# Kernel optimization log

Hardware: AMD Instinct MI355X
Metric: run time of the kernel (lower is better)

Reference implementation:

```python
import jax, jax.numpy as jnp
import numpy as np

# Module hyperparameters (from init_kwargs)
K = 1.0                       # init_curvature (registered buffer, non-trainable)
HOPFIELD_DIM = 64
BETA = 1.0 / np.sqrt(float(HOPFIELD_DIM))  # beta=None default -> 1/sqrt(d_h)
EPS = 1e-7

# ---- Lorentz / hyperboloid ops (geoopt conventions, curvature param k>0) ----

def _to_tangent0(x):
    # x: (..., d) Euclidean -> (..., d+1) in T_0 H via [0, x], norm-clipped to 3.5
    zeros = jnp.zeros(x.shape[:-1] + (1,), x.dtype)
    x = jnp.concatenate([zeros, x], axis=-1)
    n = jnp.linalg.norm(x, axis=-1, keepdims=True)
    factor = jnp.minimum(3.5 / (n + 1e-7), 1.0)
    return x * factor

def expmap0(x_euc):
    # (..., d) Euclidean -> (..., d+1) on hyperboloid via Exp_0([0, x])
    u = _to_tangent0(x_euc)
    x = u[..., 1:]
    sqrtk = jnp.sqrt(K)
    xn = jnp.maximum(jnp.linalg.norm(x, axis=-1, keepdims=True), EPS)
    theta = xn / sqrtk
    return jnp.concatenate(
        [sqrtk * jnp.cosh(theta), sqrtk * jnp.sinh(theta) * x / xn], axis=-1)

def logmap0(y):
    # (..., d+1) on hyperboloid -> (..., d) tangent at origin (spatial part)
    sqrtk = jnp.sqrt(K)
    y0 = y[..., :1]
    yr = y[..., 1:]
    yn = jnp.maximum(jnp.linalg.norm(yr, axis=-1, keepdims=True), EPS)
    d = sqrtk * jnp.arccosh(jnp.maximum(y0 / sqrtk, 1.0 + EPS))
    return d * yr / yn

def minkowski_inner(u, v):
    # <u,v>_L = -u0 v0 + sum_i u_i v_i ; returns (...) without last dim
    return -u[..., 0] * v[..., 0] + jnp.sum(u[..., 1:] * v[..., 1:], axis=-1)

# ---- KFCore forward ----

def _kfcore(queries, keys, values, Wq, bq, Wk, bk, Wv, bv):
    sqrtk = jnp.sqrt(K)
    Qe = queries @ Wq.T + bq                     # (B,S,d_h)
    Ke = keys @ Wk.T + bk                        # (B,M,d_h)
    Ve = (values @ Wk.T + bk) @ Wv.T + bv        # (B,M,d_out)
    Q = expmap0(Qe)                              # (B,S,d+1)
    Kh = expmap0(Ke)                             # (B,M,d+1)
    V = expmap0(Ve)                              # (B,M,d+1)

    dp1 = Q.shape[-1]
    sign = jnp.concatenate([-jnp.ones((1,), Q.dtype), jnp.ones((dp1 - 1,), Q.dtype)])

    # Minkowski inner pairwise: (B,S,M)
    sims = jnp.einsum('bsd,bmd->bsm', Q * sign, Kh)
    alpha = jax.nn.softmax(-BETA * sims, axis=-1)          # (B,S,M)

    # Karcher flow: tangent_mean = sum_m alpha * logmap_Q(V_m)
    # logmap_x(y) = dist(x,y) * (y + (<x,y>/k) x) / ||y + (<x,y>/k) x||_L
    ip = jnp.einsum('bsd,bmd->bsm', Q * sign, V)           # <Q_s, V_m>_L
    dist = sqrtk * jnp.arccosh(jnp.maximum(-ip / K, 1.0 + EPS))
    qq = minkowski_inner(Q, Q)[:, :, None]                 # (B,S,1)
    vv = minkowski_inner(V, V)[:, None, :]                 # (B,1,M)
    c = ip / K
    nomin_sq = vv + 2.0 * c * ip + c * c * qq              # ||nomin||_L^2, (B,S,M)
    denom = jnp.sqrt(jnp.maximum(nomin_sq, EPS))
    w = alpha * dist / denom                               # (B,S,M)
    # sum_m w * (V_m + c * Q_s)  -- avoids the (B,S,M,d+1) logmap tensor
    tm = jnp.einsum('bsm,bmd->bsd', w, V) \
         + jnp.sum(w * c, axis=-1, keepdims=True) * Q      # (B,S,d+1)

    # expmap_Q(tm) = cosh(||tm||/sqrtk) Q + sqrtk sinh(||tm||/sqrtk) tm/||tm||
    un = jnp.sqrt(jnp.maximum(minkowski_inner(tm, tm), EPS))[..., None]
    th = un / sqrtk
    z = jnp.cosh(th) * Q + sqrtk * jnp.sinh(th) * tm / un
    return logmap0(z)                                      # (B,S,d_out)


def setup_inputs() -> dict:
    key = jax.random.key(0)
    ks = jax.random.split(key, 9)
    B, S, M = 2, 2048, 4096
    SD, MD, DH, DO = 256, 256, 64, 64
    sq = 1.0 / np.sqrt(SD)
    sm = 1.0 / np.sqrt(MD)
    sh = 1.0 / np.sqrt(DH)
    return {
        'queries': jax.random.normal(ks[0], (B, S, SD), jnp.float32),
        'keys':    jax.random.normal(ks[1], (B, M, MD), jnp.float32),
        'values':  jax.random.normal(ks[2], (B, M, MD), jnp.float32),
        'Wq': jax.random.normal(ks[3], (DH, SD), jnp.float32) * sq,
        'bq': jax.random.normal(ks[4], (DH,), jnp.float32) * sq,
        'Wk': jax.random.normal(ks[5], (DH, MD), jnp.float32) * sm,
        'bk': jax.random.normal(ks[6], (DH,), jnp.float32) * sm,
        'Wv': jax.random.normal(ks[7], (DO, DH), jnp.float32) * sh,
        'bv': jax.random.normal(ks[8], (DO,), jnp.float32) * sh,
    }


def reference(queries, keys, values, Wq, bq, Wk, bk, Wv, bv):
    return _kfcore(queries, keys, values, Wq, bq, Wk, bk, Wv, bv)
```

## Files before the change

### kernel.cpp

```cpp
#include <hip/hip_runtime.h>
#include <math.h>

#define BETA  0.125f
#define SHIFT 30.0f
#define EPSF  1e-7f

typedef __attribute__((ext_vector_type(8))) short short8;
typedef __attribute__((ext_vector_type(4))) short short4v;
typedef __attribute__((ext_vector_type(4))) float f32x4;

__device__ __forceinline__ unsigned short bf16_rne(float x) {
  unsigned int u = __float_as_uint(x);
  return (unsigned short)((u + 0x7fffu + ((u >> 16) & 1u)) >> 16);
}
__device__ __forceinline__ float bf16_tof(unsigned short h) {
  return __uint_as_float(((unsigned int)h) << 16);
}
__device__ __forceinline__ void split2(float x, unsigned short& h, unsigned short& l) {
  unsigned int u = __float_as_uint(x);
  unsigned int hr = (u + 0x7fffu + ((u >> 16) & 1u)) & 0xffff0000u;
  h = (unsigned short)(hr >> 16);
  l = bf16_rne(x - __uint_as_float(hr));
}

#define ZERO_F4 68608

__global__ __launch_bounds__(256) void proj_kernel(
    const float* __restrict__ Xq, const float* __restrict__ Xk,
    const float* __restrict__ Xv,
    const float* __restrict__ Wq, const float* __restrict__ bq,
    const float* __restrict__ Wk, const float* __restrict__ bk,
    const float* __restrict__ Wv, const float* __restrict__ bv,
    float* __restrict__ Q0, float* __restrict__ K0, float* __restrict__ V0,
    unsigned short* __restrict__ Qh, unsigned short* __restrict__ Ql,
    unsigned short* __restrict__ Kh, unsigned short* __restrict__ Kl,
    unsigned short* __restrict__ Vh, unsigned short* __restrict__ Vl,
    unsigned short* __restrict__ Vth, unsigned short* __restrict__ Vtl,
    float* __restrict__ zeroRegion)
{
  __shared__ float Xs[64 * 64];
  __shared__ float Ws[64 * 64];
  __shared__ unsigned int Tr[64 * 65];

  const int bid = blockIdx.x;
  const int tid = threadIdx.x;

  {
    int idx = bid * 256 + tid;
    if (idx < ZERO_F4)
      *(float4*)&zeroRegion[idx * 4] = make_float4(0.f, 0.f, 0.f, 0.f);
  }

  const float *X, *W, *bias;
  float* y0;
  unsigned short *yh, *yl;
  bool dbl;
  int rowBase;
  if (bid < 128)      { X = Xv; W = Wk; bias = bk; y0 = V0; yh = Vh; yl = Vl; rowBase = bid << 6;         dbl = true;  }
  else if (bid < 256) { X = Xk; W = Wk; bias = bk; y0 = K0; yh = Kh; yl = Kl; rowBase = (bid - 128) << 6; dbl = false; }
  else                { X = Xq; W = Wq; bias = bq; y0 = Q0; yh = Qh; yl = Ql; rowBase = (bid - 256) << 6; dbl = false; }

  const int ty = tid >> 4, tx = tid & 15;
  const int ty4 = ty << 2, tx4 = tx << 2;

  float acc[4][4];
#pragma unroll
  for (int j = 0; j < 4; ++j) {
    float bj = bias[tx4 + j];
#pragma unroll
    for (int i = 0; i < 4; ++i) acc[i][j] = bj;
  }

  for (int kc = 0; kc < 4; ++kc) {
#pragma unroll
    for (int q = 0; q < 4; ++q) {
      int f = tid + (q << 8);
      int r = f >> 4, g = f & 15;
      int sw = (r << 6) + ((g ^ (r >> 2)) << 2);
      *(float4*)&Xs[sw] = *(const float4*)&X[(rowBase + r) * 256 + (kc << 6) + (g << 2)];
      *(float4*)&Ws[sw] = *(const float4*)&W[r * 256 + (kc << 6) + (g << 2)];
    }
    __syncthreads();
#pragma unroll 4
    for (int kk = 0; kk < 64; kk += 4) {
      const int gk = kk >> 2;
      float4 xa[4], wb[4];
#pragma unroll
      for (int i = 0; i < 4; ++i)
        xa[i] = *(const float4*)&Xs[((ty4 + i) << 6) + ((gk ^ ty) << 2)];
#pragma unroll
      for (int j = 0; j < 4; ++j)
        wb[j] = *(const float4*)&Ws[((tx4 + j) << 6) + ((gk ^ tx) << 2)];
#pragma unroll
      for (int i = 0; i < 4; ++i)
#pragma unroll
        for (int j = 0; j < 4; ++j)
          acc[i][j] += xa[i].x * wb[j].x + xa[i].y * wb[j].y +
                       xa[i].z * wb[j].z + xa[i].w * wb[j].w;
    }
    __syncthreads();
  }

  if (dbl) {
#pragma unroll
    for (int i = 0; i < 4; ++i) {
      float4 v = make_float4(acc[i][0], acc[i][1], acc[i][2], acc[i][3]);
      *(float4*)&Xs[((ty4 + i) << 6) + ((tx ^ ty) << 2)] = v;
    }
#pragma unroll
    for (int q = 0; q < 4; ++q) {
      int f = tid + (q << 8);
      int r = f >> 4, g = f & 15;
      int sw = (r << 6) + ((g ^ (r >> 2)) << 2);
      *(float4*)&Ws[sw] = *(const float4*)&Wv[(r << 6) + (g << 2)];
    }
#pragma unroll
    for (int j = 0; j < 4; ++j) {
      float bj = bv[tx4 + j];
#pragma unroll
      for (int i = 0; i < 4; ++i) acc[i][j] = bj;
    }
    __syncthreads();
#pragma unroll 4
    for (int kk = 0; kk < 64; kk += 4) {
      const int gk = kk >> 2;
      float4 xa[4], wb[4];
#pragma unroll
      for (int i = 0; i < 4; ++i)
        xa[i] = *(const float4*)&Xs[((ty4 + i) << 6) + ((gk ^ ty) << 2)];
#pragma unroll
      for (int j = 0; j < 4; ++j)
        wb[j] = *(const float4*)&Ws[((tx4 + j) << 6) + ((gk ^ tx) << 2)];
#pragma unroll
      for (int i = 0; i < 4; ++i)
#pragma unroll
        for (int j = 0; j < 4; ++j)
          acc[i][j] += xa[i].x * wb[j].x + xa[i].y * wb[j].y +
                       xa[i].z * wb[j].z + xa[i].w * wb[j].w;
    }
  }

  float n2p[4];
#pragma unroll
  for (int i = 0; i < 4; ++i)
    n2p[i] = acc[i][0] * acc[i][0] + acc[i][1] * acc[i][1] +
             acc[i][2] * acc[i][2] + acc[i][3] * acc[i][3];
#pragma unroll
  for (int i = 0; i < 4; ++i) {
    n2p[i] += __shfl_xor(n2p[i], 1);
    n2p[i] += __shfl_xor(n2p[i], 2);
    n2p[i] += __shfl_xor(n2p[i], 4);
    n2p[i] += __shfl_xor(n2p[i], 8);
  }
  unsigned short hv[4][4], lv[4][4];
#pragma unroll
  for (int i = 0; i < 4; ++i) {
    float n = sqrtf(n2p[i]);
    float factor = fminf(3.5f / (n + EPSF), 1.0f);
    float xn = fmaxf(n * factor, EPSF);
    float et = __expf(xn);
    float rt = __builtin_amdgcn_rcpf(et);
    float ch = 0.5f * (et + rt);
    float sh = 0.5f * (et - rt);
    float scale = sh * factor * __builtin_amdgcn_rcpf(xn);
    int row = rowBase + ty4 + i;
    if (tx == 0) y0[row] = ch;
#pragma unroll
    for (int j = 0; j < 4; ++j) split2(acc[i][j] * scale, hv[i][j], lv[i][j]);
    unsigned int* ph = (unsigned int*)(yh + row * 64 + tx4);
    ph[0] = (unsigned int)hv[i][0] | ((unsigned int)hv[i][1] << 16);
    ph[1] = (unsigned int)hv[i][2] | ((unsigned int)hv[i][3] << 16);
    unsigned int* pl = (unsigned int*)(yl + row * 64 + tx4);
    pl[0] = (unsigned int)lv[i][0] | ((unsigned int)lv[i][1] << 16);
    pl[1] = (unsigned int)lv[i][2] | ((unsigned int)lv[i][3] << 16);
  }

  if (dbl) {
#pragma unroll
    for (int i = 0; i < 4; ++i)
#pragma unroll
      for (int j = 0; j < 4; ++j)
        Tr[(ty4 + i) * 65 + tx4 + j] = (unsigned int)hv[i][j];
    __syncthreads();
#pragma unroll
    for (int q = 0; q < 2; ++q) {
      int f = tid + (q << 8);
      int d = f >> 3;
      int seg = (f & 7) << 3;
      unsigned int o[4];
#pragma unroll
      for (int k = 0; k < 4; ++k)
        o[k] = Tr[(seg + 2 * k) * 65 + d] | (Tr[(seg + 2 * k + 1) * 65 + d] << 16);
      *(uint4*)&Vth[d * 8192 + rowBase + seg] = make_uint4(o[0], o[1], o[2], o[3]);
    }
    __syncthreads();
#pragma unroll
    for (int i = 0; i < 4; ++i)
#pragma unroll
      for (int j = 0; j < 4; ++j)
        Tr[(ty4 + i) * 65 + tx4 + j] = (unsigned int)lv[i][j];
    __syncthreads();
#pragma unroll
    for (int q = 0; q < 2; ++q) {
      int f = tid + (q << 8);
      int d = f >> 3;
      int seg = (f & 7) << 3;
      unsigned int o[4];
#pragma unroll
      for (int k = 0; k < 4; ++k)
        o[k] = Tr[(seg + 2 * k) * 65 + d] | (Tr[(seg + 2 * k + 1) * 65 + d] << 16);
      *(uint4*)&Vtl[d * 8192 + rowBase + seg] = make_uint4(o[0], o[1], o[2], o[3]);
    }
  }
}

__global__ void __attribute__((amdgpu_waves_per_eu(4)))
__launch_bounds__(256) attn_kernel(
    const float* __restrict__ Q0g, const unsigned short* __restrict__ Qh,
    const unsigned short* __restrict__ Ql,
    const float* __restrict__ K0g, const unsigned short* __restrict__ Khg,
    const unsigned short* __restrict__ Klg,
    const float* __restrict__ V0g, const unsigned short* __restrict__ Vhg,
    const unsigned short* __restrict__ Vlg,
    const unsigned short* __restrict__ Vthg, const unsigned short* __restrict__ Vtlg,
    float* __restrict__ Tacc, float* __restrict__ T0acc,
    float* __restrict__ Lacc, float* __restrict__ WCacc)
{
  __shared__ unsigned short LB[16640];

  const int tid = threadIdx.x;
  const int wave = tid >> 6, lane = tid & 63;
  const int lm = lane & 15;
  const int lg = lane >> 4;
  const int bid = blockIdx.x;
  const int slice = bid & 15;
  const int t = bid >> 4;
  const int b = t >> 5;
  const int sT = t & 31;
  const int sBase = b * 2048 + sT * 64 + wave * 16;

  unsigned short* wbase = LB + 14336 + wave * 576;

  short8 qf[2][2];
#pragma unroll
  for (int ks = 0; ks < 2; ++ks) {
    int idx = (sBase + lm) * 64 + ks * 32 + lg * 8;
    qf[ks][0] = *(const short8*)(Qh + idx);
    qf[ks][1] = *(const short8*)(Ql + idx);
  }
  float q0r[4];
#pragma unroll
  for (int r = 0; r < 4; ++r) q0r[r] = Q0g[sBase + lg * 4 + r];

  f32x4 accT[4];
  float Lp[4], WCp[4], T0p[4];
#pragma unroll
  for (int r = 0; r < 4; ++r) { Lp[r] = 0.f; WCp[r] = 0.f; T0p[r] = 0.f; }
#pragma unroll
  for (int dj = 0; dj < 4; ++dj) accT[dj] = f32x4{0.f, 0.f, 0.f, 0.f};

  const int mSliceBase = b * 4096 + slice * 256;
  const int srow = tid >> 3;
  const int sc8 = (tid & 7) << 3;
  const int drow = tid >> 2;
  const int dseg = (tid & 3) << 3;

  for (int mc = 0; mc < 8; ++mc) {
    const int mCh = mSliceBase + (mc << 5);

    {
      int goff = (mCh + srow) * 64 + sc8;
      int loff = srow * 72 + sc8;
      *(uint4*)&LB[loff]         = *(const uint4*)&Khg[goff];
      *(uint4*)&LB[2304 + loff]  = *(const uint4*)&Klg[goff];
      *(uint4*)&LB[4608 + loff]  = *(const uint4*)&Vhg[goff];
      *(uint4*)&LB[6912 + loff]  = *(const uint4*)&Vlg[goff];
      int gofft = drow * 8192 + mCh + dseg;
      int lofft = drow * 40 + dseg;
      *(uint4*)&LB[9216 + lofft]  = *(const uint4*)&Vthg[gofft];
      *(uint4*)&LB[11776 + lofft] = *(const uint4*)&Vtlg[gofft];
    }
    float k0r[2], v0r[2];
#pragma unroll
    for (int mj = 0; mj < 2; ++mj) {
      k0r[mj] = K0g[mCh + mj * 16 + lm];
      v0r[mj] = V0g[mCh + mj * 16 + lm];
    }
    __syncthreads();

#pragma unroll
    for (int mj = 0; mj < 2; ++mj) {
      f32x4 sims = f32x4{0.f, 0.f, 0.f, 0.f};
      f32x4 ipv  = f32x4{0.f, 0.f, 0.f, 0.f};
#pragma unroll
      for (int ks = 0; ks < 2; ++ks) {
        int off = (mj * 16 + lm) * 72 + ks * 32 + lg * 8;
        short8 kh = *(const short8*)&LB[off];
        short8 kl = *(const short8*)&LB[2304 + off];
        short8 vh = *(const short8*)&LB[4608 + off];
        short8 vl = *(const short8*)&LB[6912 + off];
        sims = __builtin_amdgcn_mfma_f32_16x16x32_bf16(qf[ks][0], kh, sims, 0, 0, 0);
        sims = __builtin_amdgcn_mfma_f32_16x16x32_bf16(qf[ks][0], kl, sims, 0, 0, 0);
        sims = __builtin_amdgcn_mfma_f32_16x16x32_bf16(qf[ks][1], kh, sims, 0, 0, 0);
        ipv  = __builtin_amdgcn_mfma_f32_16x16x32_bf16(qf[ks][0], vh, ipv, 0, 0, 0);
        ipv  = __builtin_amdgcn_mfma_f32_16x16x32_bf16(qf[ks][0], vl, ipv, 0, 0, 0);
        ipv  = __builtin_amdgcn_mfma_f32_16x16x32_bf16(qf[ks][1], vh, ipv, 0, 0, 0);
      }
#pragma unroll
      for (int r = 0; r < 4; ++r) {
        float c  = ipv[r]  - q0r[r] * v0r[mj];
        float sm = sims[r] - q0r[r] * k0r[mj];
        float x = -c;
        float s2 = fmaxf(fmaf(x, x, -1.0f), EPSF);
        float rs = __builtin_amdgcn_rsqf(s2);
        float dist = __logf(fmaf(s2, rs, x));
        float e = __expf(fmaf(-BETA, sm, -SHIFT));
        float w = e * dist * rs;
        unsigned short wu = bf16_rne(w);
        float wb = bf16_tof(wu);
        Lp[r]  += e;
        WCp[r] += wb * c;
        T0p[r] += wb * v0r[mj];
        wbase[(lg * 4 + r) * 36 + mj * 16 + lm] = wu;
      }
    }

    {
      const unsigned short* p = wbase + lm * 36 + lg * 8;
      short4v a0 = *(const short4v*)p;
      short4v a1 = *(const short4v*)(p + 4);
      short8 wa = __builtin_shufflevector(a0, a1, 0, 1, 2, 3, 4, 5, 6, 7);
#pragma unroll
      for (int dj = 0; dj < 4; ++dj) {
        int off = (dj * 16 + lm) * 40 + lg * 8;
        short8 th = *(const short8*)&LB[9216 + off];
        short8 tl = *(const short8*)&LB[11776 + off];
        accT[dj] = __builtin_amdgcn_mfma_f32_16x16x32_bf16(wa, th, accT[dj], 0, 0, 0);
        accT[dj] = __builtin_amdgcn_mfma_f32_16x16x32_bf16(wa, tl, accT[dj], 0, 0, 0);
      }
    }
    __syncthreads();
  }

#pragma unroll
  for (int r = 0; r < 4; ++r)
#pragma unroll
    for (int off = 1; off < 16; off <<= 1) {
      Lp[r]  += __shfl_xor(Lp[r], off);
      WCp[r] += __shfl_xor(WCp[r], off);
      T0p[r] += __shfl_xor(T0p[r], off);
    }

#pragma unroll
  for (int r = 0; r < 4; ++r) {
    int row = sBase + lg * 4 + r;
#pragma unroll
    for (int dj = 0; dj < 4; ++dj)
      unsafeAtomicAdd(&Tacc[row * 64 + dj * 16 + lm], accT[dj][r]);
    if (lm == 0) {
      unsafeAtomicAdd(&Lacc[row],  Lp[r]);
      unsafeAtomicAdd(&WCacc[row], WCp[r]);
      unsafeAtomicAdd(&T0acc[row], T0p[r]);
    }
  }
}

__global__ __launch_bounds__(256) void combine_kernel(
    const float* __restrict__ Q0, const unsigned short* __restrict__ Qh,
    const unsigned short* __restrict__ Ql,
    const float* __restrict__ Tacc, const float* __restrict__ T0acc,
    const float* __restrict__ Lacc, const float* __restrict__ WCacc,
    float* __restrict__ out)
{
  int wid = (blockIdx.x << 2) + (threadIdx.x >> 6);
  int lane = threadIdx.x & 63;

  int qi = wid * 64 + lane;
  float Tsum = Tacc[qi];
  float T0 = T0acc[wid];
  float L  = Lacc[wid];
  float WC = WCacc[wid];

  float qd = bf16_tof(Qh[qi]) + bf16_tof(Ql[qi]);
  float q0 = Q0[wid];
  float invL = 1.0f / L;
  float td = Tsum * invL;
  float t0 = T0 * invL;
  float wc = WC * invL;

  double tt = (double)td * (double)td;
#pragma unroll
  for (int off = 1; off < 64; off <<= 1) tt += __shfl_xor(tt, off);
  tt -= (double)t0 * (double)t0;
  double mk = tt + (double)wc * (double)wc;

  float un = (float)sqrt(fmax(mk, 1e-12));
  float eu = __expf(un);
  float ru = 1.0f / eu;
  float ch = 0.5f * (eu + ru);
  float shu = 0.5f * (eu - ru) / un;

  float tmd = td + wc * qd;
  float tm0 = t0 + wc * q0;
  float zd = ch * qd + shu * tmd;
  float z0 = ch * q0 + shu * tm0;

  float p2 = zd * zd;
#pragma unroll
  for (int off = 1; off < 64; off <<= 1) p2 += __shfl_xor(p2, off);
  float yn = fmaxf(sqrtf(p2), EPSF);
  float zc = fmaxf(z0, 1.0f + EPSF);
  float dl = __logf(zc + sqrtf(fmaxf(zc * zc - 1.0f, 0.f)));
  out[qi] = dl * zd / yn;
}

extern "C" void kernel_launch(void* const* d_in, const int* in_sizes, int n_in,
                              void* d_out, int out_size, void* d_ws, size_t ws_size,
                              hipStream_t stream)
{
  const float* queries = (const float*)d_in[0];
  const float* keys    = (const float*)d_in[1];
  const float* values  = (const float*)d_in[2];
  const float* Wq      = (const float*)d_in[3];
  const float* bq      = (const float*)d_in[4];
  const float* Wk      = (const float*)d_in[5];
  const float* bk      = (const float*)d_in[6];
  const float* Wv      = (const float*)d_in[7];
  const float* bv      = (const float*)d_in[8];
  float* out = (float*)d_out;
  float* ws  = (float*)d_ws;

  float* Q0 = ws;
  float* K0 = ws + 4096;
  float* V0 = ws + 12288;
  unsigned short* Qh  = (unsigned short*)(ws + 20480);
  unsigned short* Ql  = (unsigned short*)(ws + 151552);
  unsigned short* Kh  = (unsigned short*)(ws + 282624);
  unsigned short* Kl  = (unsigned short*)(ws + 544768);
  unsigned short* Vh  = (unsigned short*)(ws + 806912);
  unsigned short* Vl  = (unsigned short*)(ws + 1069056);
  unsigned short* Vth = (unsigned short*)(ws + 1331200);
  unsigned short* Vtl = (unsigned short*)(ws + 1593344);
  float* Tacc  = ws + 1855488;
  float* T0acc = ws + 2117632;
  float* Lacc  = ws + 2121728;
  float* WCacc = ws + 2125824;

  proj_kernel<<<320, 256, 0, stream>>>(queries, keys, values, Wq, bq, Wk, bk,
                                       Wv, bv, Q0, K0, V0, Qh, Ql, Kh, Kl,
                                       Vh, Vl, Vth, Vtl, Tacc);
  attn_kernel<<<1024, 256, 0, stream>>>(
      Q0, Qh, Ql, K0, Kh, Kl, V0, Vh, Vl, Vth, Vtl,
      Tacc, T0acc, Lacc, WCacc);
  combine_kernel<<<1024, 256, 0, stream>>>(
      Q0, Qh, Ql, Tacc, T0acc, Lacc, WCacc, out);
}
```

Before: 147.1 us.

## Prefetch next K/V chunk into registers while computing current chunk

Global loads for the next 32-row K/V chunk (and its k0/v0 scalars) are issued into registers right after the barrier, so their latency overlaps with the MFMA and softmax work on the current chunk. At the top of each iteration the registers are written to LDS. The per-wave weight staging stride is also widened from 36 to 40 so a single 16-byte LDS read replaces two 8-byte reads. This costs extra registers under the 4-waves-per-EU bound and slightly more LDS.

```diff
diff --git a/kernel.cpp b/kernel.cpp
--- a/kernel.cpp
+++ b/kernel.cpp
@@ -226,7 +226,7 @@
     float* __restrict__ Tacc, float* __restrict__ T0acc,
     float* __restrict__ Lacc, float* __restrict__ WCacc)
 {
-  __shared__ unsigned short LB[16640];
+  __shared__ unsigned short LB[16896];
 
   const int tid = threadIdx.x;
   const int wave = tid >> 6, lane = tid & 63;
@@ -239,7 +239,7 @@
   const int sT = t & 31;
   const int sBase = b * 2048 + sT * 64 + wave * 16;
 
-  unsigned short* wbase = LB + 14336 + wave * 576;
+  unsigned short* wbase = LB + 14336 + wave * 640;
 
   short8 qf[2][2];
 #pragma unroll
@@ -265,28 +265,49 @@
   const int drow = tid >> 2;
   const int dseg = (tid & 3) << 3;
 
+  int mCh = mSliceBase;
+  uint4 rKh, rKl, rVh, rVl, rVt0, rVt1;
+  float rk00, rk01, rv00, rv01;
+  {
+    int goff = (mCh + srow) * 64 + sc8;
+    rKh  = *(const uint4*)&Khg[goff];
+    rKl  = *(const uint4*)&Klg[goff];
+    rVh  = *(const uint4*)&Vhg[goff];
+    rVl  = *(const uint4*)&Vlg[goff];
+    int gofft = drow * 8192 + mCh + dseg;
+    rVt0 = *(const uint4*)&Vthg[gofft];
+    rVt1 = *(const uint4*)&Vtlg[gofft];
+    rk00 = K0g[mCh + lm];      rk01 = K0g[mCh + 16 + lm];
+    rv00 = V0g[mCh + lm];      rv01 = V0g[mCh + 16 + lm];
+  }
+
   for (int mc = 0; mc < 8; ++mc) {
-    const int mCh = mSliceBase + (mc << 5);
-
     {
+      int loff = srow * 72 + sc8;
+      *(uint4*)&LB[loff]          = rKh;
+      *(uint4*)&LB[2304 + loff]   = rKl;
+      *(uint4*)&LB[4608 + loff]   = rVh;
+      *(uint4*)&LB[6912 + loff]   = rVl;
+      int lofft = drow * 40 + dseg;
+      *(uint4*)&LB[9216 + lofft]  = rVt0;
+      *(uint4*)&LB[11776 + lofft] = rVt1;
+    }
+    const float k0c0 = rk00, k0c1 = rk01, v0c0 = rv00, v0c1 = rv01;
+    __syncthreads();
+
+    if (mc < 7) {
+      mCh += 32;
       int goff = (mCh + srow) * 64 + sc8;
-      int loff = srow * 72 + sc8;
-      *(uint4*)&LB[loff]         = *(const uint4*)&Khg[goff];
-      *(uint4*)&LB[2304 + loff]  = *(const uint4*)&Klg[goff];
-      *(uint4*)&LB[4608 + loff]  = *(const uint4*)&Vhg[goff];
-      *(uint4*)&LB[6912 + loff]  = *(const uint4*)&Vlg[goff];
+      rKh  = *(const uint4*)&Khg[goff];
+      rKl  = *(const uint4*)&Klg[goff];
+      rVh  = *(const uint4*)&Vhg[goff];
+      rVl  = *(const uint4*)&Vlg[goff];
       int gofft = drow * 8192 + mCh + dseg;
-      int lofft = drow * 40 + dseg;
-      *(uint4*)&LB[9216 + lofft]  = *(const uint4*)&Vthg[gofft];
-      *(uint4*)&LB[11776 + lofft] = *(const uint4*)&Vtlg[gofft];
-    }
-    float k0r[2], v0r[2];
-#pragma unroll
-    for (int mj = 0; mj < 2; ++mj) {
-      k0r[mj] = K0g[mCh + mj * 16 + lm];
-      v0r[mj] = V0g[mCh + mj * 16 + lm];
-    }
-    __syncthreads();
+      rVt0 = *(const uint4*)&Vthg[gofft];
+      rVt1 = *(const uint4*)&Vtlg[gofft];
+      rk00 = K0g[mCh + lm];      rk01 = K0g[mCh + 16 + lm];
+      rv00 = V0g[mCh + lm];      rv01 = V0g[mCh + 16 + lm];
+    }
 
 #pragma unroll
     for (int mj = 0; mj < 2; ++mj) {
@@ -306,10 +327,12 @@
         ipv  = __builtin_amdgcn_mfma_f32_16x16x32_bf16(qf[ks][0], vl, ipv, 0, 0, 0);
         ipv  = __builtin_amdgcn_mfma_f32_16x16x32_bf16(qf[ks][1], vh, ipv, 0, 0, 0);
       }
+      const float k0m = mj ? k0c1 : k0c0;
+      const float v0m = mj ? v0c1 : v0c0;
 #pragma unroll
       for (int r = 0; r < 4; ++r) {
-        float c  = ipv[r]  - q0r[r] * v0r[mj];
-        float sm = sims[r] - q0r[r] * k0r[mj];
+        float c  = ipv[r]  - q0r[r] * v0m;
+        float sm = sims[r] - q0r[r] * k0m;
         float x = -c;
         float s2 = fmaxf(fmaf(x, x, -1.0f), EPSF);
         float rs = __builtin_amdgcn_rsqf(s2);
@@ -320,16 +343,13 @@
         float wb = bf16_tof(wu);
         Lp[r]  += e;
         WCp[r] += wb * c;
-        T0p[r] += wb * v0r[mj];
-        wbase[(lg * 4 + r) * 36 + mj * 16 + lm] = wu;
+        T0p[r] += wb * v0m;
+        wbase[(lg * 4 + r) * 40 + mj * 16 + lm] = wu;
       }
     }
 
     {
-      const unsigned short* p = wbase + lm * 36 + lg * 8;
-      short4v a0 = *(const short4v*)p;
-      short4v a1 = *(const short4v*)(p + 4);
-      short8 wa = __builtin_shufflevector(a0, a1, 0, 1, 2, 3, 4, 5, 6, 7);
+      short8 wa = *(const short8*)(wbase + lm * 40 + lg * 8);
 #pragma unroll
       for (int dj = 0; dj < 4; ++dj) {
         int off = (dj * 16 + lm) * 40 + lg * 8;
```

After: 151.2 us. 2.7% more time.

## Double proj block threads and shrink attention LDS to raise occupancy

Applied to the files above, without the earlier changes.

The projection kernel now launches 512 threads per block, each computing a 2x4 output tile instead of 4x4. This halves per-thread registers and work and adds more waves for latency hiding. The attention kernel's transposed-V LDS tile pitch drops from 40 to 36 shorts, which means split 8-byte stores and loads instead of 16-byte ones. The saved LDS lets waves_per_eu be raised from 4 to 5, at the risk of more LDS instructions and register pressure.

```diff
diff --git a/kernel.cpp b/kernel.cpp
--- a/kernel.cpp
+++ b/kernel.cpp
@@ -25,7 +25,7 @@
 
 #define ZERO_F4 68608
 
-__global__ __launch_bounds__(256) void proj_kernel(
+__global__ __launch_bounds__(512) void proj_kernel(
     const float* __restrict__ Xq, const float* __restrict__ Xk,
     const float* __restrict__ Xv,
     const float* __restrict__ Wq, const float* __restrict__ bq,
@@ -46,7 +46,7 @@
   const int tid = threadIdx.x;
 
   {
-    int idx = bid * 256 + tid;
+    int idx = bid * 512 + tid;
     if (idx < ZERO_F4)
       *(float4*)&zeroRegion[idx * 4] = make_float4(0.f, 0.f, 0.f, 0.f);
   }
@@ -60,21 +60,23 @@
   else if (bid < 256) { X = Xk; W = Wk; bias = bk; y0 = K0; yh = Kh; yl = Kl; rowBase = (bid - 128) << 6; dbl = false; }
   else                { X = Xq; W = Wq; bias = bq; y0 = Q0; yh = Qh; yl = Ql; rowBase = (bid - 256) << 6; dbl = false; }
 
-  const int ty = tid >> 4, tx = tid & 15;
-  const int ty4 = ty << 2, tx4 = tx << 2;
-
-  float acc[4][4];
+  const int ty = tid >> 4;
+  const int tx = tid & 15;
+  const int ty2 = ty << 1, tx4 = tx << 2;
+  const int kx = ty >> 1;
+
+  float acc[2][4];
 #pragma unroll
   for (int j = 0; j < 4; ++j) {
     float bj = bias[tx4 + j];
 #pragma unroll
-    for (int i = 0; i < 4; ++i) acc[i][j] = bj;
+    for (int i = 0; i < 2; ++i) acc[i][j] = bj;
   }
 
   for (int kc = 0; kc < 4; ++kc) {
 #pragma unroll
-    for (int q = 0; q < 4; ++q) {
-      int f = tid + (q << 8);
+    for (int q = 0; q < 2; ++q) {
+      int f = tid + (q << 9);
       int r = f >> 4, g = f & 15;
       int sw = (r << 6) + ((g ^ (r >> 2)) << 2);
       *(float4*)&Xs[sw] = *(const float4*)&X[(rowBase + r) * 256 + (kc << 6) + (g << 2)];
@@ -84,15 +86,15 @@
 #pragma unroll 4
     for (int kk = 0; kk < 64; kk += 4) {
       const int gk = kk >> 2;
-      float4 xa[4], wb[4];
-#pragma unroll
-      for (int i = 0; i < 4; ++i)
-        xa[i] = *(const float4*)&Xs[((ty4 + i) << 6) + ((gk ^ ty) << 2)];
+      float4 xa[2], wb[4];
+#pragma unroll
+      for (int i = 0; i < 2; ++i)
+        xa[i] = *(const float4*)&Xs[((ty2 + i) << 6) + ((gk ^ kx) << 2)];
 #pragma unroll
       for (int j = 0; j < 4; ++j)
         wb[j] = *(const float4*)&Ws[((tx4 + j) << 6) + ((gk ^ tx) << 2)];
 #pragma unroll
-      for (int i = 0; i < 4; ++i)
+      for (int i = 0; i < 2; ++i)
 #pragma unroll
         for (int j = 0; j < 4; ++j)
           acc[i][j] += xa[i].x * wb[j].x + xa[i].y * wb[j].y +
@@ -103,13 +105,13 @@
 
   if (dbl) {
 #pragma unroll
-    for (int i = 0; i < 4; ++i) {
+    for (int i = 0; i < 2; ++i) {
       float4 v = make_float4(acc[i][0], acc[i][1], acc[i][2], acc[i][3]);
-      *(float4*)&Xs[((ty4 + i) << 6) + ((tx ^ ty) << 2)] = v;
-    }
-#pragma unroll
-    for (int q = 0; q < 4; ++q) {
-      int f = tid + (q << 8);
+      *(float4*)&Xs[((ty2 + i) << 6) + ((tx ^ kx) << 2)] = v;
+    }
+#pragma unroll
+    for (int q = 0; q < 2; ++q) {
+      int f = tid + (q << 9);
       int r = f >> 4, g = f & 15;
       int sw = (r << 6) + ((g ^ (r >> 2)) << 2);
       *(float4*)&Ws[sw] = *(const float4*)&Wv[(r << 6) + (g << 2)];
@@ -118,21 +120,21 @@
     for (int j = 0; j < 4; ++j) {
       float bj = bv[tx4 + j];
 #pragma unroll
-      for (int i = 0; i < 4; ++i) acc[i][j] = bj;
+      for (int i = 0; i < 2; ++i) acc[i][j] = bj;
     }
     __syncthreads();
 #pragma unroll 4
     for (int kk = 0; kk < 64; kk += 4) {
       const int gk = kk >> 2;
-      float4 xa[4], wb[4];
-#pragma unroll
-      for (int i = 0; i < 4; ++i)
-        xa[i] = *(const float4*)&Xs[((ty4 + i) << 6) + ((gk ^ ty) << 2)];
+      float4 xa[2], wb[4];
+#pragma unroll
+      for (int i = 0; i < 2; ++i)
+        xa[i] = *(const float4*)&Xs[((ty2 + i) << 6) + ((gk ^ kx) << 2)];
 #pragma unroll
       for (int j = 0; j < 4; ++j)
         wb[j] = *(const float4*)&Ws[((tx4 + j) << 6) + ((gk ^ tx) << 2)];
 #pragma unroll
-      for (int i = 0; i < 4; ++i)
+      for (int i = 0; i < 2; ++i)
 #pragma unroll
         for (int j = 0; j < 4; ++j)
           acc[i][j] += xa[i].x * wb[j].x + xa[i].y * wb[j].y +
@@ -140,21 +142,21 @@
     }
   }
 
-  float n2p[4];
-#pragma unroll
-  for (int i = 0; i < 4; ++i)
+  float n2p[2];
+#pragma unroll
+  for (int i = 0; i < 2; ++i)
     n2p[i] = acc[i][0] * acc[i][0] + acc[i][1] * acc[i][1] +
              acc[i][2] * acc[i][2] + acc[i][3] * acc[i][3];
 #pragma unroll
-  for (int i = 0; i < 4; ++i) {
+  for (int i = 0; i < 2; ++i) {
     n2p[i] += __shfl_xor(n2p[i], 1);
     n2p[i] += __shfl_xor(n2p[i], 2);
     n2p[i] += __shfl_xor(n2p[i], 4);
     n2p[i] += __shfl_xor(n2p[i], 8);
   }
-  unsigned short hv[4][4], lv[4][4];
-#pragma unroll
-  for (int i = 0; i < 4; ++i) {
+  unsigned short hv[2][4], lv[2][4];
+#pragma unroll
+  for (int i = 0; i < 2; ++i) {
     float n = sqrtf(n2p[i]);
     float factor = fminf(3.5f / (n + EPSF), 1.0f);
     float xn = fmaxf(n * factor, EPSF);
@@ -163,7 +165,7 @@
     float ch = 0.5f * (et + rt);
     float sh = 0.5f * (et - rt);
     float scale = sh * factor * __builtin_amdgcn_rcpf(xn);
-    int row = rowBase + ty4 + i;
+    int row = rowBase + ty2 + i;
     if (tx == 0) y0[row] = ch;
 #pragma unroll
     for (int j = 0; j < 4; ++j) split2(acc[i][j] * scale, hv[i][j], lv[i][j]);
@@ -177,14 +179,13 @@
 
   if (dbl) {
 #pragma unroll
-    for (int i = 0; i < 4; ++i)
+    for (int i = 0; i < 2; ++i)
 #pragma unroll
       for (int j = 0; j < 4; ++j)
-        Tr[(ty4 + i) * 65 + tx4 + j] = (unsigned int)hv[i][j];
-    __syncthreads();
-#pragma unroll
-    for (int q = 0; q < 2; ++q) {
-      int f = tid + (q << 8);
+        Tr[(ty2 + i) * 65 + tx4 + j] = (unsigned int)hv[i][j];
+    __syncthreads();
+    {
+      int f = tid;
       int d = f >> 3;
       int seg = (f & 7) << 3;
       unsigned int o[4];
@@ -195,14 +196,13 @@
     }
     __syncthreads();
 #pragma unroll
-    for (int i = 0; i < 4; ++i)
+    for (int i = 0; i < 2; ++i)
 #pragma unroll
       for (int j = 0; j < 4; ++j)
-        Tr[(ty4 + i) * 65 + tx4 + j] = (unsigned int)lv[i][j];
-    __syncthreads();
-#pragma unroll
-    for (int q = 0; q < 2; ++q) {
-      int f = tid + (q << 8);
+        Tr[(ty2 + i) * 65 + tx4 + j] = (unsigned int)lv[i][j];
+    __syncthreads();
+    {
+      int f = tid;
       int d = f >> 3;
       int seg = (f & 7) << 3;
       unsigned int o[4];
@@ -214,7 +214,7 @@
   }
 }
 
-__global__ void __attribute__((amdgpu_waves_per_eu(4)))
+__global__ void __attribute__((amdgpu_waves_per_eu(5)))
 __launch_bounds__(256) attn_kernel(
     const float* __restrict__ Q0g, const unsigned short* __restrict__ Qh,
     const unsigned short* __restrict__ Ql,
@@ -226,7 +226,7 @@
     float* __restrict__ Tacc, float* __restrict__ T0acc,
     float* __restrict__ Lacc, float* __restrict__ WCacc)
 {
-  __shared__ unsigned short LB[16640];
+  __shared__ unsigned short LB[16128];
 
   const int tid = threadIdx.x;
   const int wave = tid >> 6, lane = tid & 63;
@@ -239,7 +239,7 @@
   const int sT = t & 31;
   const int sBase = b * 2048 + sT * 64 + wave * 16;
 
-  unsigned short* wbase = LB + 14336 + wave * 576;
+  unsigned short* wbase = LB + 13824 + wave * 576;
 
   short8 qf[2][2];
 #pragma unroll
@@ -276,9 +276,13 @@
       *(uint4*)&LB[4608 + loff]  = *(const uint4*)&Vhg[goff];
       *(uint4*)&LB[6912 + loff]  = *(const uint4*)&Vlg[goff];
       int gofft = drow * 8192 + mCh + dseg;
-      int lofft = drow * 40 + dseg;
-      *(uint4*)&LB[9216 + lofft]  = *(const uint4*)&Vthg[gofft];
-      *(uint4*)&LB[11776 + lofft] = *(const uint4*)&Vtlg[gofft];
+      int lofft = drow * 36 + dseg;
+      uint4 vt0 = *(const uint4*)&Vthg[gofft];
+      uint4 vt1 = *(const uint4*)&Vtlg[gofft];
+      *(uint2*)&LB[9216 + lofft]      = make_uint2(vt0.x, vt0.y);
+      *(uint2*)&LB[9216 + lofft + 4]  = make_uint2(vt0.z, vt0.w);
+      *(uint2*)&LB[11520 + lofft]     = make_uint2(vt1.x, vt1.y);
+      *(uint2*)&LB[11520 + lofft + 4] = make_uint2(vt1.z, vt1.w);
     }
     float k0r[2], v0r[2];
 #pragma unroll
@@ -326,15 +330,22 @@
     }
 
     {
-      const unsigned short* p = wbase + lm * 36 + lg * 8;
-      short4v a0 = *(const short4v*)p;
-      short4v a1 = *(const short4v*)(p + 4);
-      short8 wa = __builtin_shufflevector(a0, a1, 0, 1, 2, 3, 4, 5, 6, 7);
+      short8 wa;
+      {
+        const unsigned short* p = wbase + lm * 36 + lg * 8;
+        short4v a0 = *(const short4v*)p;
+        short4v a1 = *(const short4v*)(p + 4);
+        wa = __builtin_shufflevector(a0, a1, 0, 1, 2, 3, 4, 5, 6, 7);
+      }
 #pragma unroll
       for (int dj = 0; dj < 4; ++dj) {
-        int off = (dj * 16 + lm) * 40 + lg * 8;
-        short8 th = *(const short8*)&LB[9216 + off];
-        short8 tl = *(const short8*)&LB[11776 + off];
+        int off = (dj * 16 + lm) * 36 + lg * 8;
+        short4v h0 = *(const short4v*)&LB[9216 + off];
+        short4v h1 = *(const short4v*)&LB[9216 + off + 4];
+        short4v l0 = *(const short4v*)&LB[11520 + off];
+        short4v l1 = *(const short4v*)&LB[11520 + off + 4];
+        short8 th = __builtin_shufflevector(h0, h1, 0, 1, 2, 3, 4, 5, 6, 7);
+        short8 tl = __builtin_shufflevector(l0, l1, 0, 1, 2, 3, 4, 5, 6, 7);
         accT[dj] = __builtin_amdgcn_mfma_f32_16x16x32_bf16(wa, th, accT[dj], 0, 0, 0);
         accT[dj] = __builtin_amdgcn_mfma_f32_16x16x32_bf16(wa, tl, accT[dj], 0, 0, 0);
       }
@@ -446,7 +457,7 @@
   float* Lacc  = ws + 2121728;
   float* WCacc = ws + 2125824;
 
-  proj_kernel<<<320, 256, 0, stream>>>(queries, keys, values, Wq, bq, Wk, bk,
+  proj_kernel<<<320, 512, 0, stream>>>(queries, keys, values, Wq, bq, Wk, bk,
                                        Wv, bv, Q0, K0, V0, Qh, Ql, Kh, Kl,
                                        Vh, Vl, Vth, Vtl, Tacc);
   attn_kernel<<<1024, 256, 0, stream>>>(
```

Result: slower. 161.5 us (+9.8%).

## Rewrite projection GEMMs with split-bf16 MFMA instead of FP32 SIMT

Applied to the files above, without the earlier changes.

Replaces the FP32 shared-memory tiled SIMT matmul in the projection kernel with MFMA 16x16x32 bf16 instructions. Operands are split into hi/lo bf16 parts and combined in three MFMAs to approximate fp32 accuracy. X and W fragments now load straight from global memory without LDS staging, and the second Wv projection round-trips through a small per-wave LDS buffer. This trades the FP32 ALU work for matrix-core throughput, at some accuracy risk from dropping the lo*lo term and with less coalesced global loads.

```diff
diff --git a/kernel.cpp b/kernel.cpp
--- a/kernel.cpp
+++ b/kernel.cpp
@@ -21,6 +21,17 @@
   unsigned int hr = (u + 0x7fffu + ((u >> 16) & 1u)) & 0xffff0000u;
   h = (unsigned short)(hr >> 16);
   l = bf16_rne(x - __uint_as_float(hr));
+}
+__device__ __forceinline__ void split8(float4 a, float4 b, short8& h8, short8& l8) {
+  unsigned short h, l;
+  split2(a.x, h, l); h8[0] = (short)h; l8[0] = (short)l;
+  split2(a.y, h, l); h8[1] = (short)h; l8[1] = (short)l;
+  split2(a.z, h, l); h8[2] = (short)h; l8[2] = (short)l;
+  split2(a.w, h, l); h8[3] = (short)h; l8[3] = (short)l;
+  split2(b.x, h, l); h8[4] = (short)h; l8[4] = (short)l;
+  split2(b.y, h, l); h8[5] = (short)h; l8[5] = (short)l;
+  split2(b.z, h, l); h8[6] = (short)h; l8[6] = (short)l;
+  split2(b.w, h, l); h8[7] = (short)h; l8[7] = (short)l;
 }
 
 #define ZERO_F4 68608
@@ -38,9 +49,8 @@
     unsigned short* __restrict__ Vth, unsigned short* __restrict__ Vtl,
     float* __restrict__ zeroRegion)
 {
-  __shared__ float Xs[64 * 64];
-  __shared__ float Ws[64 * 64];
   __shared__ unsigned int Tr[64 * 65];
+  __shared__ unsigned short VkL[4][2][16 * 72];
 
   const int bid = blockIdx.x;
   const int tid = threadIdx.x;
@@ -60,102 +70,99 @@
   else if (bid < 256) { X = Xk; W = Wk; bias = bk; y0 = K0; yh = Kh; yl = Kl; rowBase = (bid - 128) << 6; dbl = false; }
   else                { X = Xq; W = Wq; bias = bq; y0 = Q0; yh = Qh; yl = Ql; rowBase = (bid - 256) << 6; dbl = false; }
 
-  const int ty = tid >> 4, tx = tid & 15;
-  const int ty4 = ty << 2, tx4 = tx << 2;
-
-  float acc[4][4];
-#pragma unroll
-  for (int j = 0; j < 4; ++j) {
-    float bj = bias[tx4 + j];
-#pragma unroll
-    for (int i = 0; i < 4; ++i) acc[i][j] = bj;
-  }
-
-  for (int kc = 0; kc < 4; ++kc) {
-#pragma unroll
-    for (int q = 0; q < 4; ++q) {
-      int f = tid + (q << 8);
-      int r = f >> 4, g = f & 15;
-      int sw = (r << 6) + ((g ^ (r >> 2)) << 2);
-      *(float4*)&Xs[sw] = *(const float4*)&X[(rowBase + r) * 256 + (kc << 6) + (g << 2)];
-      *(float4*)&Ws[sw] = *(const float4*)&W[r * 256 + (kc << 6) + (g << 2)];
-    }
-    __syncthreads();
-#pragma unroll 4
-    for (int kk = 0; kk < 64; kk += 4) {
-      const int gk = kk >> 2;
-      float4 xa[4], wb[4];
-#pragma unroll
-      for (int i = 0; i < 4; ++i)
-        xa[i] = *(const float4*)&Xs[((ty4 + i) << 6) + ((gk ^ ty) << 2)];
-#pragma unroll
-      for (int j = 0; j < 4; ++j)
-        wb[j] = *(const float4*)&Ws[((tx4 + j) << 6) + ((gk ^ tx) << 2)];
-#pragma unroll
-      for (int i = 0; i < 4; ++i)
-#pragma unroll
-        for (int j = 0; j < 4; ++j)
-          acc[i][j] += xa[i].x * wb[j].x + xa[i].y * wb[j].y +
-                       xa[i].z * wb[j].z + xa[i].w * wb[j].w;
-    }
-    __syncthreads();
+  const int wave = tid >> 6, lane = tid & 63;
+  const int lm = lane & 15;
+  const int lg = lane >> 4;
+  const int rowB = rowBase + (wave << 4);
+
+  short8 Ah[8], Al[8];
+  {
+    const float* Xr = X + (rowB + lm) * 256 + lg * 8;
+#pragma unroll
+    for (int ks = 0; ks < 8; ++ks) {
+      float4 x0 = *(const float4*)&Xr[ks * 32];
+      float4 x1 = *(const float4*)&Xr[ks * 32 + 4];
+      split8(x0, x1, Ah[ks], Al[ks]);
+    }
+  }
+
+  f32x4 acc[4];
+#pragma unroll
+  for (int nj = 0; nj < 4; ++nj) {
+    float b = bias[nj * 16 + lm];
+    acc[nj] = f32x4{b, b, b, b};
+  }
+#pragma unroll
+  for (int nj = 0; nj < 4; ++nj) {
+    const float* Wr = W + (nj * 16 + lm) * 256 + lg * 8;
+#pragma unroll
+    for (int ks = 0; ks < 8; ++ks) {
+      float4 w0 = *(const float4*)&Wr[ks * 32];
+      float4 w1 = *(const float4*)&Wr[ks * 32 + 4];
+      short8 Bh, Bl;
+      split8(w0, w1, Bh, Bl);
+      acc[nj] = __builtin_amdgcn_mfma_f32_16x16x32_bf16(Ah[ks], Bh, acc[nj], 0, 0, 0);
+      acc[nj] = __builtin_amdgcn_mfma_f32_16x16x32_bf16(Ah[ks], Bl, acc[nj], 0, 0, 0);
+      acc[nj] = __builtin_amdgcn_mfma_f32_16x16x32_bf16(Al[ks], Bh, acc[nj], 0, 0, 0);
+    }
   }
 
   if (dbl) {
-#pragma unroll
-    for (int i = 0; i < 4; ++i) {
-      float4 v = make_float4(acc[i][0], acc[i][1], acc[i][2], acc[i][3]);
-      *(float4*)&Xs[((ty4 + i) << 6) + ((tx ^ ty) << 2)] = v;
-    }
-#pragma unroll
-    for (int q = 0; q < 4; ++q) {
-      int f = tid + (q << 8);
-      int r = f >> 4, g = f & 15;
-      int sw = (r << 6) + ((g ^ (r >> 2)) << 2);
-      *(float4*)&Ws[sw] = *(const float4*)&Wv[(r << 6) + (g << 2)];
-    }
-#pragma unroll
-    for (int j = 0; j < 4; ++j) {
-      float bj = bv[tx4 + j];
-#pragma unroll
-      for (int i = 0; i < 4; ++i) acc[i][j] = bj;
-    }
-    __syncthreads();
-#pragma unroll 4
-    for (int kk = 0; kk < 64; kk += 4) {
-      const int gk = kk >> 2;
-      float4 xa[4], wb[4];
-#pragma unroll
-      for (int i = 0; i < 4; ++i)
-        xa[i] = *(const float4*)&Xs[((ty4 + i) << 6) + ((gk ^ ty) << 2)];
-#pragma unroll
-      for (int j = 0; j < 4; ++j)
-        wb[j] = *(const float4*)&Ws[((tx4 + j) << 6) + ((gk ^ tx) << 2)];
-#pragma unroll
-      for (int i = 0; i < 4; ++i)
-#pragma unroll
-        for (int j = 0; j < 4; ++j)
-          acc[i][j] += xa[i].x * wb[j].x + xa[i].y * wb[j].y +
-                       xa[i].z * wb[j].z + xa[i].w * wb[j].w;
+    unsigned short* vh_ = &VkL[wave][0][0];
+    unsigned short* vl_ = &VkL[wave][1][0];
+#pragma unroll
+    for (int nj = 0; nj < 4; ++nj)
+#pragma unroll
+      for (int r = 0; r < 4; ++r) {
+        unsigned short h, l;
+        split2(acc[nj][r], h, l);
+        vh_[(lg * 4 + r) * 72 + nj * 16 + lm] = h;
+        vl_[(lg * 4 + r) * 72 + nj * 16 + lm] = l;
+      }
+    __syncthreads();
+    short8 A2h[2], A2l[2];
+#pragma unroll
+    for (int ks = 0; ks < 2; ++ks) {
+      A2h[ks] = *(const short8*)&vh_[lm * 72 + ks * 32 + lg * 8];
+      A2l[ks] = *(const short8*)&vl_[lm * 72 + ks * 32 + lg * 8];
+    }
+#pragma unroll
+    for (int nj = 0; nj < 4; ++nj) {
+      float b = bv[nj * 16 + lm];
+      acc[nj] = f32x4{b, b, b, b};
+    }
+#pragma unroll
+    for (int nj = 0; nj < 4; ++nj) {
+      const float* Wr = Wv + (nj * 16 + lm) * 64 + lg * 8;
+#pragma unroll
+      for (int ks = 0; ks < 2; ++ks) {
+        float4 w0 = *(const float4*)&Wr[ks * 32];
+        float4 w1 = *(const float4*)&Wr[ks * 32 + 4];
+        short8 Bh, Bl;
+        split8(w0, w1, Bh, Bl);
+        acc[nj] = __builtin_amdgcn_mfma_f32_16x16x32_bf16(A2h[ks], Bh, acc[nj], 0, 0, 0);
+        acc[nj] = __builtin_amdgcn_mfma_f32_16x16x32_bf16(A2h[ks], Bl, acc[nj], 0, 0, 0);
+        acc[nj] = __builtin_amdgcn_mfma_f32_16x16x32_bf16(A2l[ks], Bh, acc[nj], 0, 0, 0);
+      }
     }
   }
 
   float n2p[4];
 #pragma unroll
-  for (int i = 0; i < 4; ++i)
-    n2p[i] = acc[i][0] * acc[i][0] + acc[i][1] * acc[i][1] +
-             acc[i][2] * acc[i][2] + acc[i][3] * acc[i][3];
-#pragma unroll
-  for (int i = 0; i < 4; ++i) {
-    n2p[i] += __shfl_xor(n2p[i], 1);
-    n2p[i] += __shfl_xor(n2p[i], 2);
-    n2p[i] += __shfl_xor(n2p[i], 4);
-    n2p[i] += __shfl_xor(n2p[i], 8);
+  for (int r = 0; r < 4; ++r)
+    n2p[r] = acc[0][r] * acc[0][r] + acc[1][r] * acc[1][r] +
+             acc[2][r] * acc[2][r] + acc[3][r] * acc[3][r];
+#pragma unroll
+  for (int r = 0; r < 4; ++r) {
+    n2p[r] += __shfl_xor(n2p[r], 1);
+    n2p[r] += __shfl_xor(n2p[r], 2);
+    n2p[r] += __shfl_xor(n2p[r], 4);
+    n2p[r] += __shfl_xor(n2p[r], 8);
   }
   unsigned short hv[4][4], lv[4][4];
 #pragma unroll
-  for (int i = 0; i < 4; ++i) {
-    float n = sqrtf(n2p[i]);
+  for (int r = 0; r < 4; ++r) {
+    float n = sqrtf(n2p[r]);
     float factor = fminf(3.5f / (n + EPSF), 1.0f);
     float xn = fmaxf(n * factor, EPSF);
     float et = __expf(xn);
@@ -163,24 +170,22 @@
     float ch = 0.5f * (et + rt);
     float sh = 0.5f * (et - rt);
     float scale = sh * factor * __builtin_amdgcn_rcpf(xn);
-    int row = rowBase + ty4 + i;
-    if (tx == 0) y0[row] = ch;
-#pragma unroll
-    for (int j = 0; j < 4; ++j) split2(acc[i][j] * scale, hv[i][j], lv[i][j]);
-    unsigned int* ph = (unsigned int*)(yh + row * 64 + tx4);
-    ph[0] = (unsigned int)hv[i][0] | ((unsigned int)hv[i][1] << 16);
-    ph[1] = (unsigned int)hv[i][2] | ((unsigned int)hv[i][3] << 16);
-    unsigned int* pl = (unsigned int*)(yl + row * 64 + tx4);
-    pl[0] = (unsigned int)lv[i][0] | ((unsigned int)lv[i][1] << 16);
-    pl[1] = (unsigned int)lv[i][2] | ((unsigned int)lv[i][3] << 16);
+    int row = rowB + lg * 4 + r;
+    if (lm == 0) y0[row] = ch;
+#pragma unroll
+    for (int nj = 0; nj < 4; ++nj) {
+      split2(acc[nj][r] * scale, hv[r][nj], lv[r][nj]);
+      yh[row * 64 + nj * 16 + lm] = hv[r][nj];
+      yl[row * 64 + nj * 16 + lm] = lv[r][nj];
+    }
   }
 
   if (dbl) {
 #pragma unroll
-    for (int i = 0; i < 4; ++i)
-#pragma unroll
-      for (int j = 0; j < 4; ++j)
-        Tr[(ty4 + i) * 65 + tx4 + j] = (unsigned int)hv[i][j];
+    for (int r = 0; r < 4; ++r)
+#pragma unroll
+      for (int nj = 0; nj < 4; ++nj)
+        Tr[(wave * 16 + lg * 4 + r) * 65 + nj * 16 + lm] = (unsigned int)hv[r][nj];
     __syncthreads();
 #pragma unroll
     for (int q = 0; q < 2; ++q) {
@@ -195,10 +200,10 @@
     }
     __syncthreads();
 #pragma unroll
-    for (int i = 0; i < 4; ++i)
-#pragma unroll
-      for (int j = 0; j < 4; ++j)
-        Tr[(ty4 + i) * 65 + tx4 + j] = (unsigned int)lv[i][j];
+    for (int r = 0; r < 4; ++r)
+#pragma unroll
+      for (int nj = 0; nj < 4; ++nj)
+        Tr[(wave * 16 + lg * 4 + r) * 65 + nj * 16 + lm] = (unsigned int)lv[r][nj];
     __syncthreads();
 #pragma unroll
     for (int q = 0; q < 2; ++q) {
@@ -326,10 +331,13 @@
     }
 
     {
-      const unsigned short* p = wbase + lm * 36 + lg * 8;
-      short4v a0 = *(const short4v*)p;
-      short4v a1 = *(const short4v*)(p + 4);
-      short8 wa = __builtin_shufflevector(a0, a1, 0, 1, 2, 3, 4, 5, 6, 7);
+      short8 wa;
+      {
+        const unsigned short* p = wbase + lm * 36 + lg * 8;
+        short4v a0 = *(const short4v*)p;
+        short4v a1 = *(const short4v*)(p + 4);
+        wa = __builtin_shufflevector(a0, a1, 0, 1, 2, 3, 4, 5, 6, 7);
+      }
 #pragma unroll
       for (int dj = 0; dj < 4; ++dj) {
         int off = (dj * 16 + lm) * 40 + lg * 8;
```

New measurement: 144.6 us. Within noise of the previous version (-1.7%).
